# Kernel optimization log

Measured on AMD Instinct MI355X. Metric: run time of the kernel, lower is better.

The kernel has to match this reference:

```python
import jax, jax.numpy as jnp
import numpy as np

D_MODEL = 1024
N_HEADS = 16


def setup_inputs() -> dict:
    key = jax.random.key(0)
    ks = jax.random.split(key, 7)
    scale = 1.0 / np.sqrt(D_MODEL)
    seq = jax.random.normal(ks[0], (4, 1024, D_MODEL), dtype=jnp.float32)
    Wq = jax.random.normal(ks[1], (D_MODEL, D_MODEL), dtype=jnp.float32) * scale
    bq = jax.random.normal(ks[2], (D_MODEL,), dtype=jnp.float32) * 0.02
    Wk = jax.random.normal(ks[3], (D_MODEL, D_MODEL), dtype=jnp.float32) * scale
    bk = jax.random.normal(ks[4], (D_MODEL,), dtype=jnp.float32) * 0.02
    Wv = jax.random.normal(ks[5], (D_MODEL, D_MODEL), dtype=jnp.float32) * scale
    bv = jax.random.normal(ks[6], (D_MODEL,), dtype=jnp.float32) * 0.02
    return {"seq": seq, "Wq": Wq, "bq": bq, "Wk": Wk, "bk": bk, "Wv": Wv, "bv": bv}


def reference(seq, Wq, bq, Wk, bk, Wv, bv):
    B, S, D = seq.shape
    H = N_HEADS
    dv = D // H
    # nn.Linear: x @ W.T + b; W stored [out, in]
    q = (seq @ Wq.T + bq).reshape(B, S, H, dv).transpose(0, 2, 1, 3)  # [B,H,S,dv]
    k = (seq @ Wk.T + bk).reshape(B, S, H, dv).transpose(0, 2, 1, 3)
    v = (seq @ Wv.T + bv).reshape(B, S, H, dv).transpose(0, 2, 1, 3)
    scores = jnp.einsum('bhqd,bhkd->bhqk', q, k) / jnp.sqrt(jnp.asarray(dv, seq.dtype))
    p = jax.nn.softmax(scores, axis=-1)
    out = jnp.einsum('bhqk,bhkd->bhqd', p, v)  # [B,H,S,dv]
    return out.transpose(0, 2, 1, 3).reshape(B, S, D)
```

## Files before the change

### kernel.cpp

```cpp
#include <hip/hip_runtime.h>
#include <hip/hip_fp16.h>

typedef _Float16 f16x8 __attribute__((ext_vector_type(8)));
typedef _Float16 f16x4 __attribute__((ext_vector_type(4)));
typedef float f32x4 __attribute__((ext_vector_type(4)));
typedef float f32x16 __attribute__((ext_vector_type(16)));

#define D_MODEL 1024
#define SEQ 1024
#define BATCH 4
#define NH 16
#define DV 64
#define M_TOTAL (BATCH * SEQ)
#define QBLK 128

__device__ __forceinline__ void gload16(const _Float16* g, _Float16* lds) {
    __builtin_amdgcn_global_load_lds((const __attribute__((address_space(1))) void*)g,
                                     (__attribute__((address_space(3))) void*)lds,
                                     16, 0, 0);
}

__global__ void cvt_f32_f16(const float* __restrict__ s, _Float16* __restrict__ d, int n) {
    int i = (blockIdx.x * blockDim.x + threadIdx.x) * 8;
    if (i >= n) return;
    float4 a = *(const float4*)(s + i);
    float4 b = *(const float4*)(s + i + 4);
    f16x8 h;
    h[0] = (_Float16)a.x; h[1] = (_Float16)a.y; h[2] = (_Float16)a.z; h[3] = (_Float16)a.w;
    h[4] = (_Float16)b.x; h[5] = (_Float16)b.y; h[6] = (_Float16)b.z; h[7] = (_Float16)b.w;
    *(f16x8*)(d + i) = h;
}

__global__ void cvt3_f32_f16(const float* __restrict__ s0, const float* __restrict__ s1,
                             const float* __restrict__ s2, _Float16* __restrict__ d0,
                             _Float16* __restrict__ d1, _Float16* __restrict__ d2, int n) {
    const float* s = (blockIdx.y == 0) ? s0 : (blockIdx.y == 1 ? s1 : s2);
    _Float16*    d = (blockIdx.y == 0) ? d0 : (blockIdx.y == 1 ? d1 : d2);
    int i = (blockIdx.x * blockDim.x + threadIdx.x) * 8;
    if (i >= n) return;
    float4 a = *(const float4*)(s + i);
    float4 b = *(const float4*)(s + i + 4);
    f16x8 h;
    h[0] = (_Float16)a.x; h[1] = (_Float16)a.y; h[2] = (_Float16)a.z; h[3] = (_Float16)a.w;
    h[4] = (_Float16)b.x; h[5] = (_Float16)b.y; h[6] = (_Float16)b.z; h[7] = (_Float16)b.w;
    *(f16x8*)(d + i) = h;
}

__global__ __launch_bounds__(512, 2) void qkv_gemm(
    const _Float16* __restrict__ X,
    const _Float16* __restrict__ W0, const _Float16* __restrict__ W1, const _Float16* __restrict__ W2,
    const float* __restrict__ b0, const float* __restrict__ b1, const float* __restrict__ b2,
    _Float16* __restrict__ Qo, _Float16* __restrict__ Ko, _Float16* __restrict__ Vto)
{
    __shared__ _Float16 SM[4 * 256 * 64];
#define ABASE(buf) (SM + (buf) * 16384)
#define BBASE(buf) (SM + 32768 + (buf) * 16384)

    const int tid = threadIdx.x;
    const int l = tid & 63;
    const int w = tid >> 6;
    const int wr = w >> 2, wc = w & 3;

    const int bid = blockIdx.x;
    const int nid = (bid & 7) * 24 + (bid >> 3);
    const int mt = nid & 15, ntg = nid >> 4;
    const int mat = ntg >> 2, nt = ntg & 3;
    const _Float16* Wm  = (mat == 0) ? W0 : (mat == 1 ? W1 : W2);
    const float*    bia = (mat == 0) ? b0 : (mat == 1 ? b1 : b2);
    const int m0 = mt * 256, n0 = nt * 256;

    const int str = tid >> 3;
    const int sc8 = ((tid & 7) ^ (str & 7)) * 8;
    const _Float16* xsrc = X  + (size_t)(m0 + str) * D_MODEL + sc8;
    const _Float16* wsrc = Wm + (size_t)(n0 + str) * D_MODEL + sc8;
    const int ldst = str * 64 + (tid & 7) * 8;

#define SA(buf, kt, h) do { \
    gload16(xsrc + (size_t)((h) * 128) * D_MODEL + (kt) * 64, ABASE(buf) + (h) * 8192 + ldst); \
    gload16(xsrc + (size_t)((h) * 128 + 64) * D_MODEL + (kt) * 64, ABASE(buf) + (h) * 8192 + 4096 + ldst); } while (0)
#define SB(buf, kt, h) do { \
    gload16(wsrc + (size_t)((h) * 128) * D_MODEL + (kt) * 64, BBASE(buf) + (h) * 8192 + ldst); \
    gload16(wsrc + (size_t)((h) * 128 + 64) * D_MODEL + (kt) * 64, BBASE(buf) + (h) * 8192 + 4096 + ldst); } while (0)

    const int fr = l & 15, g = l >> 4, fr7 = l & 7;
    const int wrow = wr * 128, bcol = wc * 64;

    f32x4 acc[8][4] = {};
    f16x8 b[4][2];

    SB(0, 0, 0); SB(0, 0, 1);
    SA(0, 0, 0); SA(0, 0, 1);
    SB(1, 1, 0); SB(1, 1, 1);
    asm volatile("s_waitcnt vmcnt(4)" ::: "memory");
    __builtin_amdgcn_s_barrier();

#define PHASES(BUF, TSA_BUF, TSA, TSB_BUF, TSB)                                              \
    _Pragma("unroll")                                                                        \
    for (int p = 0; p < 4; ++p) {                                                            \
        if (p == 0) {                                                                        \
            _Pragma("unroll")                                                                \
            for (int nj = 0; nj < 4; ++nj) {                                                 \
                const int rb = (bcol + nj * 16 + fr) * 64;                                   \
                b[nj][0] = *(const f16x8*)&BBASE(BUF)[rb + ((g ^ fr7) << 3)];                \
                b[nj][1] = *(const f16x8*)&BBASE(BUF)[rb + (((4 + g) ^ fr7) << 3)];          \
            }                                                                                \
        }                                                                                    \
        f16x8 aq[2][2];                                                                      \
        _Pragma("unroll")                                                                    \
        for (int q = 0; q < 2; ++q) {                                                        \
            const int ra = (wrow + (2 * p + q) * 16 + fr) * 64;                              \
            aq[q][0] = *(const f16x8*)&ABASE(BUF)[ra + ((g ^ fr7) << 3)];                    \
            aq[q][1] = *(const f16x8*)&ABASE(BUF)[ra + (((4 + g) ^ fr7) << 3)];              \
        }                                                                                    \
        if (p == 0) SA(TSA_BUF, TSA, 0);                                                     \
        else if (p == 1) SA(TSA_BUF, TSA, 1);                                                \
        else if (p == 2) SB(TSB_BUF, TSB, 0);                                                \
        else SB(TSB_BUF, TSB, 1);                                                            \
        __builtin_amdgcn_s_barrier();                                                        \
        __builtin_amdgcn_s_setprio(1);                                                       \
        _Pragma("unroll")                                                                    \
        for (int ks = 0; ks < 2; ++ks)                                                       \
            _Pragma("unroll")                                                                \
            for (int q = 0; q < 2; ++q)                                                      \
                _Pragma("unroll")                                                            \
                for (int nj = 0; nj < 4; ++nj)                                               \
                    acc[2 * p + q][nj] = __builtin_amdgcn_mfma_f32_16x16x32_f16(             \
                        aq[q][ks], b[nj][ks], acc[2 * p + q][nj], 0, 0, 0);                  \
        __builtin_amdgcn_s_setprio(0);                                                       \
        if (p == 3) asm volatile("s_waitcnt vmcnt(4)" ::: "memory");                         \
        __builtin_amdgcn_s_barrier();                                                        \
    }

    for (int it = 0; it < 8; ++it) {
        const int tA = 2 * it + 1;
        const int tN = (2 * it + 2 < 16) ? 2 * it + 2 : 15;
        const int tM = (2 * it + 3 < 16) ? 2 * it + 3 : 15;
        PHASES(0, 1, tA, 0, tN)
        PHASES(1, 0, tN, 1, tM)
    }
#undef PHASES
#undef SA
#undef SB

    if (mat != 2) {
        const float scale = (mat == 0) ? 0.125f * 1.44269504088896340736f : 1.0f;
#pragma unroll
        for (int nj = 0; nj < 4; ++nj) {
            const int o = n0 + bcol + nj * 16 + fr;
            const float bb = bia[o];
            const int h = o >> 6, dd = o & 63;
#pragma unroll
            for (int mi = 0; mi < 8; ++mi) {
#pragma unroll
                for (int r = 0; r < 4; ++r) {
                    const int m = m0 + wrow + mi * 16 + g * 4 + r;
                    const int bi = m >> 10, s = m & 1023;
                    const float v = (acc[mi][nj][r] + bb) * scale;
                    const _Float16 hv = (_Float16)v;
                    const int bh = bi * NH + h;
                    if (mat == 0) Qo[((size_t)bh * SEQ + s) * DV + dd] = hv;
                    else          Ko[((size_t)bh * SEQ + s) * DV + dd] = hv;
                }
            }
        }
    } else {
        asm volatile("s_waitcnt vmcnt(0)" ::: "memory");
        __syncthreads();
#pragma unroll
        for (int nj = 0; nj < 4; ++nj) {
            const int n = bcol + nj * 16 + fr;
            const float bb = bia[n0 + n];
#pragma unroll
            for (int mi = 0; mi < 8; ++mi) {
#pragma unroll
                for (int r = 0; r < 4; ++r) {
                    const int m = wrow + mi * 16 + g * 4 + r;
                    SM[n * 256 + ((((m >> 3) + n) & 31) << 3) + (m & 7)] =
                        (_Float16)(acc[mi][nj][r] + bb);
                }
            }
        }
        __syncthreads();
        const int bi = m0 >> 10, s0 = m0 & 1023;
#pragma unroll
        for (int itp = 0; itp < 16; ++itp) {
            const int task = itp * 512 + tid;
            const int dd = task >> 5, sc = task & 31;
            f16x8 vv = *(const f16x8*)&SM[dd * 256 + (((sc + dd) & 31) << 3)];
            const int og = n0 + dd;
            const int h = og >> 6, d = og & 63;
            const int bh = bi * NH + h;
            *(f16x8*)(Vto + ((size_t)bh * DV + d) * SEQ + s0 + sc * 8) = vv;
        }
    }
#undef ABASE
#undef BBASE
}

__global__ __launch_bounds__(256, 2) void attn(
    const _Float16* __restrict__ Q, const _Float16* __restrict__ K,
    const _Float16* __restrict__ Vt, float* __restrict__ out)
{
    __shared__ _Float16 Kb[2][64 * 64];
    __shared__ _Float16 Vb[2][64 * 64];

    const int tid = threadIdx.x;
    const int w = tid >> 6, l = tid & 63;
    const int q_ = l & 31, hl = l >> 5;

    const int fid = blockIdx.y * 8 + blockIdx.x;
    const int nid = (fid & 7) * 64 + (fid >> 3);
    const int bh = nid >> 3, qt = nid & 7;
    const int b = bh >> 4, h = bh & 15;
    const int q0 = qt * QBLK + w * 32;

    const int str = tid >> 3;
    const int scs = ((tid & 7) ^ (str & 7)) * 8;
    const int ldst = str * 64 + (tid & 7) * 8;
    const _Float16* Kg = K  + (size_t)bh * SEQ * DV;
    const _Float16* Vg = Vt + (size_t)bh * DV * SEQ;

    f16x8 qf[4];
    {
        const _Float16* qp = Q + ((size_t)bh * SEQ + q0 + q_) * DV + hl * 8;
#pragma unroll
        for (int c = 0; c < 4; ++c) qf[c] = *(const f16x8*)(qp + c * 16);
    }

    float m_run = -1e30f, l_run = 0.f;
    f32x16 acc0 = {}, acc1 = {};

#define STAGE(buf, kt) do {                                                              \
        gload16(Kg + (size_t)((kt) * 64 + str) * DV + scs, &Kb[buf][0] + ldst);          \
        gload16(Kg + (size_t)((kt) * 64 + str + 32) * DV + scs, &Kb[buf][32 * 64] + ldst);\
        gload16(Vg + (size_t)str * SEQ + (kt) * 64 + scs, &Vb[buf][0] + ldst);           \
        gload16(Vg + (size_t)(str + 32) * SEQ + (kt) * 64 + scs, &Vb[buf][32 * 64] + ldst);\
    } while (0)

#define QK(S, ct, kt) do {                                                               \
        S = (f32x16){};                                                                  \
        const int row = (kt) * 32 + q_;                                                  \
        _Pragma("unroll")                                                                \
        for (int c = 0; c < 4; ++c) {                                                    \
            f16x8 kf = *(const f16x8*)&Kb[ct][row * 64 + (((c * 2 + hl) ^ (row & 7)) << 3)]; \
            S = __builtin_amdgcn_mfma_f32_32x32x16_f16(kf, qf[c], S, 0, 0, 0);           \
        }                                                                                \
    } while (0)

#define SMPV(S, ct, kt) do {                                                             \
        float lmax = S[0];                                                               \
        _Pragma("unroll")                                                                \
        for (int r = 1; r < 16; ++r) lmax = fmaxf(lmax, S[r]);                           \
        const float mm = fmaxf(lmax, __shfl_xor(lmax, 32));                              \
        if (!__all(mm - m_run <= 8.0f)) {                                                \
            const float mn = fmaxf(m_run, mm);                                           \
            const float al = exp2f(m_run - mn);                                          \
            l_run *= al;                                                                 \
            acc0 *= al; acc1 *= al;                                                      \
            m_run = mn;                                                                  \
        }                                                                                \
        float p[16];                                                                     \
        float rsum = 0.f;                                                                \
        _Pragma("unroll")                                                                \
        for (int r = 0; r < 16; ++r) { p[r] = exp2f(S[r] - m_run); rsum += p[r]; }       \
        l_run += rsum;                                                                   \
        f16x4 pf[4];                                                                     \
        _Pragma("unroll")                                                                \
        for (int G = 0; G < 4; ++G) {                                                    \
            pf[G][0] = (_Float16)p[4 * G];     pf[G][1] = (_Float16)p[4 * G + 1];        \
            pf[G][2] = (_Float16)p[4 * G + 2]; pf[G][3] = (_Float16)p[4 * G + 3];        \
        }                                                                                \
        __builtin_amdgcn_s_setprio(1);                                                   \
        _Pragma("unroll")                                                                \
        for (int G = 0; G < 4; ++G) {                                                    \
            const int c16 = (kt) * 4 + G;                                                \
            const int r0 = q_;                                                           \
            f16x4 v0 = *(const f16x4*)&Vb[ct][r0 * 64 + (((c16) ^ (r0 & 7)) << 3) + hl * 4]; \
            acc0 = __builtin_amdgcn_mfma_f32_32x32x8f16(v0, pf[G], acc0, 0, 0, 0);       \
            const int r1 = 32 + q_;                                                      \
            f16x4 v1 = *(const f16x4*)&Vb[ct][r1 * 64 + (((c16) ^ (r1 & 7)) << 3) + hl * 4]; \
            acc1 = __builtin_amdgcn_mfma_f32_32x32x8f16(v1, pf[G], acc1, 0, 0, 0);       \
        }                                                                                \
        __builtin_amdgcn_s_setprio(0);                                                   \
    } while (0)

    STAGE(0, 0);
    __syncthreads();

    for (int t = 0; t < 16; ++t) {
        const int ct = t & 1;
        if (t < 15) STAGE(ct ^ 1, t + 1);

        f32x16 s0, s1;
        QK(s0, ct, 0);
        QK(s1, ct, 1);
        SMPV(s0, ct, 0);
        SMPV(s1, ct, 1);

        __syncthreads();
    }
#undef STAGE
#undef QK
#undef SMPV

    l_run += __shfl_xor(l_run, 32);
    const float inv = 1.0f / l_run;
    float* ob = out + ((size_t)b * SEQ + q0 + q_) * D_MODEL + h * DV;
#pragma unroll
    for (int rg = 0; rg < 4; ++rg) {
        float4 v4;
        const int d0 = rg * 8 + 4 * hl;
        v4.x = acc0[4 * rg + 0] * inv; v4.y = acc0[4 * rg + 1] * inv;
        v4.z = acc0[4 * rg + 2] * inv; v4.w = acc0[4 * rg + 3] * inv;
        *(float4*)(ob + d0) = v4;
        v4.x = acc1[4 * rg + 0] * inv; v4.y = acc1[4 * rg + 1] * inv;
        v4.z = acc1[4 * rg + 2] * inv; v4.w = acc1[4 * rg + 3] * inv;
        *(float4*)(ob + 32 + d0) = v4;
    }
}

extern "C" void kernel_launch(void* const* d_in, const int* in_sizes, int n_in,
                              void* d_out, int out_size, void* d_ws, size_t ws_size,
                              hipStream_t stream) {
    const float* seq = (const float*)d_in[0];
    const float* Wq  = (const float*)d_in[1];
    const float* bq  = (const float*)d_in[2];
    const float* Wk  = (const float*)d_in[3];
    const float* bk  = (const float*)d_in[4];
    const float* Wv  = (const float*)d_in[5];
    const float* bv  = (const float*)d_in[6];
    float* out = (float*)d_out;

    _Float16* seqh = (_Float16*)d_ws;
    _Float16* wqh  = seqh + (size_t)M_TOTAL * D_MODEL;
    _Float16* wkh  = wqh + (size_t)D_MODEL * D_MODEL;
    _Float16* wvh  = wkh + (size_t)D_MODEL * D_MODEL;
    _Float16* Qh   = wvh + (size_t)D_MODEL * D_MODEL;
    _Float16* Kh   = Qh + (size_t)M_TOTAL * D_MODEL;
    _Float16* Vth  = Kh + (size_t)M_TOTAL * D_MODEL;

    const int n_seq = M_TOTAL * D_MODEL;
    const int n_w   = D_MODEL * D_MODEL;
    cvt_f32_f16<<<n_seq / (256 * 8), 256, 0, stream>>>(seq, seqh, n_seq);
    cvt3_f32_f16<<<dim3(n_w / (256 * 8), 3), 256, 0, stream>>>(Wq, Wk, Wv, wqh, wkh, wvh, n_w);

    qkv_gemm<<<192, 512, 0, stream>>>(
        seqh, wqh, wkh, wvh, bq, bk, bv, Qh, Kh, Vth);

    attn<<<dim3(SEQ / QBLK, BATCH * NH), 256, 0, stream>>>(Qh, Kh, Vth, out);
}
```

Before: 85.38 us.

## Split KV loop across two wave groups per attention block and merge in LDS

Doubles the attention block to 512 threads, with two groups of four waves each processing alternating 64-key tiles for the same 128 queries. The KV buffer grows to four slots so each group prefetches its next tile. At the end, partial softmax states and accumulators are combined through LDS reused as scratch. This halves the serial KV iterations per wave to raise latency hiding, at the cost of a merge step and more LDS per block.

```diff
diff --git a/kernel.cpp b/kernel.cpp
--- a/kernel.cpp
+++ b/kernel.cpp
@@ -197,26 +197,29 @@
 #undef BBASE
 }
 
-__global__ __launch_bounds__(256, 2) void attn(
+__global__ __launch_bounds__(512, 4) void attn(
     const _Float16* __restrict__ Q, const _Float16* __restrict__ K,
     const _Float16* __restrict__ Vt, float* __restrict__ out)
 {
-    __shared__ _Float16 Kb[2][64 * 64];
-    __shared__ _Float16 Vb[2][64 * 64];
+    __shared__ _Float16 Kb[4][64 * 64];
+    __shared__ _Float16 Vb[4][64 * 64];
 
     const int tid = threadIdx.x;
     const int w = tid >> 6, l = tid & 63;
+    const int grp = w >> 2, wl = w & 3;
     const int q_ = l & 31, hl = l >> 5;
 
     const int fid = blockIdx.y * 8 + blockIdx.x;
     const int nid = (fid & 7) * 64 + (fid >> 3);
     const int bh = nid >> 3, qt = nid & 7;
     const int b = bh >> 4, h = bh & 15;
-    const int q0 = qt * QBLK + w * 32;
-
-    const int str = tid >> 3;
-    const int scs = ((tid & 7) ^ (str & 7)) * 8;
-    const int ldst = str * 64 + (tid & 7) * 8;
+    const int q0 = qt * QBLK + wl * 32;
+
+    const int half = tid >> 8;
+    const int gt = tid & 255;
+    const int str = gt >> 3;
+    const int scs = ((gt & 7) ^ (str & 7)) * 8;
+    const int ldst = str * 64 + (gt & 7) * 8;
     const _Float16* Kg = K  + (size_t)bh * SEQ * DV;
     const _Float16* Vg = Vt + (size_t)bh * DV * SEQ;
 
@@ -230,92 +233,119 @@
     float m_run = -1e30f, l_run = 0.f;
     f32x16 acc0 = {}, acc1 = {};
 
-#define STAGE(buf, kt) do {                                                              \
-        gload16(Kg + (size_t)((kt) * 64 + str) * DV + scs, &Kb[buf][0] + ldst);          \
-        gload16(Kg + (size_t)((kt) * 64 + str + 32) * DV + scs, &Kb[buf][32 * 64] + ldst);\
-        gload16(Vg + (size_t)str * SEQ + (kt) * 64 + scs, &Vb[buf][0] + ldst);           \
-        gload16(Vg + (size_t)(str + 32) * SEQ + (kt) * 64 + scs, &Vb[buf][32 * 64] + ldst);\
+#define STAGET(T) do {                                                                    \
+        const int slot = (T) & 3;                                                         \
+        gload16(Kg + (size_t)((T) * 64 + str) * DV + scs, &Kb[slot][0] + ldst);           \
+        gload16(Kg + (size_t)((T) * 64 + str + 32) * DV + scs, &Kb[slot][32 * 64] + ldst);\
+        gload16(Vg + (size_t)str * SEQ + (T) * 64 + scs, &Vb[slot][0] + ldst);            \
+        gload16(Vg + (size_t)(str + 32) * SEQ + (T) * 64 + scs, &Vb[slot][32 * 64] + ldst);\
     } while (0)
 
-#define QK(S, ct, kt) do {                                                               \
-        S = (f32x16){};                                                                  \
-        const int row = (kt) * 32 + q_;                                                  \
-        _Pragma("unroll")                                                                \
-        for (int c = 0; c < 4; ++c) {                                                    \
-            f16x8 kf = *(const f16x8*)&Kb[ct][row * 64 + (((c * 2 + hl) ^ (row & 7)) << 3)]; \
-            S = __builtin_amdgcn_mfma_f32_32x32x16_f16(kf, qf[c], S, 0, 0, 0);           \
-        }                                                                                \
+#define QK(S, slot, kt) do {                                                              \
+        S = (f32x16){};                                                                   \
+        const int row = (kt) * 32 + q_;                                                   \
+        _Pragma("unroll")                                                                 \
+        for (int c = 0; c < 4; ++c) {                                                     \
+            f16x8 kf = *(const f16x8*)&Kb[slot][row * 64 + (((c * 2 + hl) ^ (row & 7)) << 3)]; \
+            S = __builtin_amdgcn_mfma_f32_32x32x16_f16(kf, qf[c], S, 0, 0, 0);            \
+        }                                                                                 \
     } while (0)
 
-#define SMPV(S, ct, kt) do {                                                             \
-        float lmax = S[0];                                                               \
-        _Pragma("unroll")                                                                \
-        for (int r = 1; r < 16; ++r) lmax = fmaxf(lmax, S[r]);                           \
-        const float mm = fmaxf(lmax, __shfl_xor(lmax, 32));                              \
-        if (!__all(mm - m_run <= 8.0f)) {                                                \
-            const float mn = fmaxf(m_run, mm);                                           \
-            const float al = exp2f(m_run - mn);                                          \
-            l_run *= al;                                                                 \
-            acc0 *= al; acc1 *= al;                                                      \
-            m_run = mn;                                                                  \
-        }                                                                                \
-        float p[16];                                                                     \
-        float rsum = 0.f;                                                                \
-        _Pragma("unroll")                                                                \
-        for (int r = 0; r < 16; ++r) { p[r] = exp2f(S[r] - m_run); rsum += p[r]; }       \
-        l_run += rsum;                                                                   \
-        f16x4 pf[4];                                                                     \
-        _Pragma("unroll")                                                                \
-        for (int G = 0; G < 4; ++G) {                                                    \
-            pf[G][0] = (_Float16)p[4 * G];     pf[G][1] = (_Float16)p[4 * G + 1];        \
-            pf[G][2] = (_Float16)p[4 * G + 2]; pf[G][3] = (_Float16)p[4 * G + 3];        \
-        }                                                                                \
-        __builtin_amdgcn_s_setprio(1);                                                   \
-        _Pragma("unroll")                                                                \
-        for (int G = 0; G < 4; ++G) {                                                    \
-            const int c16 = (kt) * 4 + G;                                                \
-            const int r0 = q_;                                                           \
-            f16x4 v0 = *(const f16x4*)&Vb[ct][r0 * 64 + (((c16) ^ (r0 & 7)) << 3) + hl * 4]; \
-            acc0 = __builtin_amdgcn_mfma_f32_32x32x8f16(v0, pf[G], acc0, 0, 0, 0);       \
-            const int r1 = 32 + q_;                                                      \
-            f16x4 v1 = *(const f16x4*)&Vb[ct][r1 * 64 + (((c16) ^ (r1 & 7)) << 3) + hl * 4]; \
-            acc1 = __builtin_amdgcn_mfma_f32_32x32x8f16(v1, pf[G], acc1, 0, 0, 0);       \
-        }                                                                                \
-        __builtin_amdgcn_s_setprio(0);                                                   \
+#define SMPV(S, slot, kt) do {                                                            \
+        float lmax = S[0];                                                                \
+        _Pragma("unroll")                                                                 \
+        for (int r = 1; r < 16; ++r) lmax = fmaxf(lmax, S[r]);                            \
+        const float mm = fmaxf(lmax, __shfl_xor(lmax, 32));                               \
+        if (!__all(mm - m_run <= 8.0f)) {                                                 \
+            const float mn = fmaxf(m_run, mm);                                            \
+            const float al = exp2f(m_run - mn);                                           \
+            l_run *= al;                                                                  \
+            acc0 *= al; acc1 *= al;                                                       \
+            m_run = mn;                                                                   \
+        }                                                                                 \
+        float p[16];                                                                      \
+        float rsum = 0.f;                                                                 \
+        _Pragma("unroll")                                                                 \
+        for (int r = 0; r < 16; ++r) { p[r] = exp2f(S[r] - m_run); rsum += p[r]; }        \
+        l_run += rsum;                                                                    \
+        f16x4 pf[4];                                                                      \
+        _Pragma("unroll")                                                                 \
+        for (int G = 0; G < 4; ++G) {                                                     \
+            pf[G][0] = (_Float16)p[4 * G];     pf[G][1] = (_Float16)p[4 * G + 1];         \
+            pf[G][2] = (_Float16)p[4 * G + 2]; pf[G][3] = (_Float16)p[4 * G + 3];         \
+        }                                                                                 \
+        __builtin_amdgcn_s_setprio(1);                                                    \
+        _Pragma("unroll")                                                                 \
+        for (int G = 0; G < 4; ++G) {                                                     \
+            const int c16 = (kt) * 4 + G;                                                 \
+            const int r0 = q_;                                                            \
+            f16x4 v0 = *(const f16x4*)&Vb[slot][r0 * 64 + (((c16) ^ (r0 & 7)) << 3) + hl * 4]; \
+            acc0 = __builtin_amdgcn_mfma_f32_32x32x8f16(v0, pf[G], acc0, 0, 0, 0);        \
+            const int r1 = 32 + q_;                                                       \
+            f16x4 v1 = *(const f16x4*)&Vb[slot][r1 * 64 + (((c16) ^ (r1 & 7)) << 3) + hl * 4]; \
+            acc1 = __builtin_amdgcn_mfma_f32_32x32x8f16(v1, pf[G], acc1, 0, 0, 0);        \
+        }                                                                                 \
+        __builtin_amdgcn_s_setprio(0);                                                    \
     } while (0)
 
-    STAGE(0, 0);
+    STAGET(half);
     __syncthreads();
 
-    for (int t = 0; t < 16; ++t) {
-        const int ct = t & 1;
-        if (t < 15) STAGE(ct ^ 1, t + 1);
+    for (int i = 0; i < 8; ++i) {
+        const int T = 2 * i + grp;
+        const int slot = T & 3;
+        if (i < 7) STAGET(2 * i + 2 + half);
 
         f32x16 s0, s1;
-        QK(s0, ct, 0);
-        QK(s1, ct, 1);
-        SMPV(s0, ct, 0);
-        SMPV(s1, ct, 1);
+        QK(s0, slot, 0);
+        QK(s1, slot, 1);
+        SMPV(s0, slot, 0);
+        SMPV(s1, slot, 1);
 
         __syncthreads();
     }
-#undef STAGE
+#undef STAGET
 #undef QK
 #undef SMPV
 
     l_run += __shfl_xor(l_run, 32);
-    const float inv = 1.0f / l_run;
-    float* ob = out + ((size_t)b * SEQ + q0 + q_) * D_MODEL + h * DV;
-#pragma unroll
-    for (int rg = 0; rg < 4; ++rg) {
-        float4 v4;
-        const int d0 = rg * 8 + 4 * hl;
-        v4.x = acc0[4 * rg + 0] * inv; v4.y = acc0[4 * rg + 1] * inv;
-        v4.z = acc0[4 * rg + 2] * inv; v4.w = acc0[4 * rg + 3] * inv;
-        *(float4*)(ob + d0) = v4;
-        v4.x = acc1[4 * rg + 0] * inv; v4.y = acc1[4 * rg + 1] * inv;
-        v4.z = acc1[4 * rg + 2] * inv; v4.w = acc1[4 * rg + 3] * inv;
-        *(float4*)(ob + 32 + d0) = v4;
+
+    float* Ob = (float*)&Kb[0][0];
+    float* Ml = (float*)&Vb[0][0];
+    if (grp == 1) {
+        float* dst = Ob + (wl * 64 + l) * 32;
+#pragma unroll
+        for (int r = 0; r < 16; ++r) { dst[r] = acc0[r]; dst[16 + r] = acc1[r]; }
+        if (l < 32) {
+            Ml[(wl * 32 + q_) * 2]     = m_run;
+            Ml[(wl * 32 + q_) * 2 + 1] = l_run;
+        }
+    }
+    __syncthreads();
+    if (grp == 0) {
+        const float m1 = Ml[(wl * 32 + q_) * 2];
+        const float l1 = Ml[(wl * 32 + q_) * 2 + 1];
+        const float M  = fmaxf(m_run, m1);
+        const float e0 = exp2f(m_run - M);
+        const float e1 = exp2f(m1 - M);
+        const float inv = 1.0f / (e0 * l_run + e1 * l1);
+        const float* src = Ob + (wl * 64 + l) * 32;
+        float* ob = out + ((size_t)b * SEQ + q0 + q_) * D_MODEL + h * DV;
+#pragma unroll
+        for (int rg = 0; rg < 4; ++rg) {
+            float4 v4;
+            const int d0 = rg * 8 + 4 * hl;
+            v4.x = (acc0[4 * rg + 0] * e0 + src[4 * rg + 0] * e1) * inv;
+            v4.y = (acc0[4 * rg + 1] * e0 + src[4 * rg + 1] * e1) * inv;
+            v4.z = (acc0[4 * rg + 2] * e0 + src[4 * rg + 2] * e1) * inv;
+            v4.w = (acc0[4 * rg + 3] * e0 + src[4 * rg + 3] * e1) * inv;
+            *(float4*)(ob + d0) = v4;
+            v4.x = (acc1[4 * rg + 0] * e0 + src[16 + 4 * rg + 0] * e1) * inv;
+            v4.y = (acc1[4 * rg + 1] * e0 + src[16 + 4 * rg + 1] * e1) * inv;
+            v4.z = (acc1[4 * rg + 2] * e0 + src[16 + 4 * rg + 2] * e1) * inv;
+            v4.w = (acc1[4 * rg + 3] * e0 + src[16 + 4 * rg + 3] * e1) * inv;
+            *(float4*)(ob + 32 + d0) = v4;
+        }
     }
 }
 
@@ -347,5 +377,5 @@
     qkv_gemm<<<192, 512, 0, stream>>>(
         seqh, wqh, wkh, wvh, bq, bk, bv, Qh, Kh, Vth);
 
-    attn<<<dim3(SEQ / QBLK, BATCH * NH), 256, 0, stream>>>(Qh, Kh, Vth, out);
-}
+    attn<<<dim3(SEQ / QBLK, BATCH * NH), 512, 0, stream>>>(Qh, Kh, Vth, out);
+}
```

Measured after the change: 81.87 us. -4.1%, faster.
